# Performance work log

Measured on AMD Instinct MI355X. Metric: run time of the kernel, lower is better.

Reference implementation:

```python
import jax, jax.numpy as jnp
import numpy as np

N = 100000   # nodes
D = 128      # node_dim (features == positions for radius search)
E = 1000000  # edges
EA = 16      # edge_attr dim
M = 256      # number of center points
K = 64       # max_num_neighbors
RADIUS = 16.5
THRESH = 0.1


def setup_inputs() -> dict:
    key = jax.random.key(0)
    ks = jax.random.split(key, 9)
    s = 1.0 / np.sqrt(D)
    return {
        "x": jax.random.normal(ks[0], (N, D), jnp.float32),
        "edge_index": jax.random.randint(ks[1], (2, E), 0, N, dtype=jnp.int64),
        "edge_attr": jax.random.normal(ks[2], (E, EA), jnp.float32),
        "center": jax.random.normal(ks[3], (M, D), jnp.float32),
        "W_root": jax.random.normal(ks[4], (D, D), jnp.float32) * s,
        "W_neigh": jax.random.normal(ks[5], (D, D), jnp.float32) * s,
        "W_edge": jax.random.normal(ks[6], (EA, D), jnp.float32) * (1.0 / np.sqrt(EA)),
        "lin_w": jax.random.normal(ks[7], (D, 1), jnp.float32) * s,
        "lin_b": jnp.zeros((1,), jnp.float32),
    }


def reference(x, edge_index, edge_attr, center, W_root, W_neigh, W_edge, lin_w, lin_b):
    n = x.shape[0]
    m = center.shape[0]

    # --- radius(x=k_data.x, y=center): up to K neighbors within RADIUS per center ---
    d2 = (jnp.sum(center * center, axis=1)[:, None]
          + jnp.sum(x * x, axis=1)[None, :]
          - 2.0 * (center @ x.T))                       # [M, N]
    within = d2 <= RADIUS * RADIUS
    neg = jnp.where(within, -d2, -jnp.inf)
    vals, cols = jax.lax.top_k(neg, K)                  # K nearest inside ball per center
    valid = jnp.isfinite(vals)                          # [M, K]

    # node membership from `col` (drop invalid slots via out-of-bounds index)
    cols_safe = jnp.where(valid, cols, n)
    in_nb = jnp.zeros((n,), bool).at[cols_safe.reshape(-1)].set(True, mode='drop')

    # torch.unique(stack([row, col])) mixes center (row) indices in as well:
    # a center index c < n marks node c if that center has >=1 neighbor
    has_nb = jnp.any(valid, axis=1)                     # [M]
    sel = in_nb.at[jnp.arange(m)].max(has_nb)

    # --- subgraph(col, edge_index, edge_attr): keep edges with both ends in col set ---
    src, dst = edge_index[0], edge_index[1]
    edge_keep = in_nb[src] & in_nb[dst]                 # [E]

    # --- weighting module: GraphConv on the subgraph (edge_attr-aware) ---
    msg = (x[src] @ W_neigh + edge_attr @ W_edge) * edge_keep[:, None].astype(x.dtype)
    agg = jax.ops.segment_sum(msg, dst, num_segments=n)  # [N, D]
    weighting = x @ W_root + agg

    # --- linear -> relu -> threshold gate ---
    w = jax.nn.relu(weighting @ lin_w + lin_b)[:, 0]    # [N]
    return jnp.logical_and(sel, w > THRESH)
```

## Files before the change

### kernel.cpp

```cpp
#include <hip/hip_runtime.h>
#include <stdint.h>

typedef unsigned long long u64;
typedef unsigned int u32;
typedef unsigned short u16;
typedef __attribute__((ext_vector_type(8))) short bf16x8;
typedef __attribute__((ext_vector_type(4))) float f32x4;

#define DD 128
#define EAD 16
#define R2C 272.25f
#define NBINS 4096
#define CAPB 16
#define CANDCAP 512
#define THRESHV 0.1
#define BN 128

#define NPAD 100096
#define NBLKMAX 800
#define L32_BYTES ((size_t)256 * NBLKMAX * CAPB * 4)
#define CNTB_OFF  L32_BYTES
#define CNTB_BYTES ((size_t)256 * NBLKMAX * 2)
#define DBL_OFF   (CNTB_OFF + CNTB_BYTES)
#define DU    0
#define DR    128
#define DV    256
#define DCC   272
#define DROOT 528
#define DA    (528 + NPAD)
#define DAGG  (528 + 2*NPAD)
#define DEND  (528 + 3*NPAD)
#define INT_OFF (DBL_OFF + (size_t)DEND * 8)
#define CCT_B   0
#define MASK_B  2048
#define HNB_B   (2048 + 12800)
#define OVF_B   (2048 + 12800 + 1024)
#define INT_BYTES (2048 + 12800 + 1024 + 1024)
#define BF_OFF   (INT_OFF + INT_BYTES)
#define XX_OFF   (BF_OFF + 2*(size_t)256*128*2)
#define ZERO_OFF   (DBL_OFF + (size_t)DAGG * 8)
#define ZERO_BYTES ((size_t)NPAD * 8 + INT_BYTES)
#define WS_NEED    (XX_OFF + (size_t)NPAD * 4)

__device__ __forceinline__ float fma4(float4 a, float4 b, float acc) {
  acc = fmaf(a.x, b.x, acc); acc = fmaf(a.y, b.y, acc);
  acc = fmaf(a.z, b.z, acc); acc = fmaf(a.w, b.w, acc);
  return acc;
}

__device__ __forceinline__ short f2bf(float f) {
  u32 u = __float_as_uint(f);
  u32 r = (u + 0x7fffu + ((u >> 16) & 1u)) >> 16;
  return (short)r;
}
__device__ __forceinline__ float bf2f(short h) {
  return __uint_as_float(((u32)(unsigned short)h) << 16);
}

__device__ float d2f32(const float* __restrict__ center, const float* __restrict__ x,
                       int c, int n, float ccv) {
  float dt = 0.f, xx = 0.f;
  for (int j = 0; j < DD; j += 4) {
    float4 xv = *(const float4*)(x + (size_t)n*DD + j);
    float4 cv = *(const float4*)(center + (size_t)c*DD + j);
    dt = fma4(xv, cv, dt); xx = fma4(xv, xv, xx);
  }
  return (ccv + xx) - 2.0f*dt;
}

__global__ void ka_pre(const float* __restrict__ Wr, const float* __restrict__ Wn,
                       const float* __restrict__ We, const float* __restrict__ lw,
                       const float* __restrict__ center,
                       double* __restrict__ dbl, float2* __restrict__ cct,
                       short* __restrict__ chi, short* __restrict__ clo, int M) {
  int t = threadIdx.x;
  if (blockIdx.x == 0) {
    if (t < DD) {
      double su = 0.0, sr = 0.0;
      for (int j = 0; j < DD; ++j) {
        double l = (double)lw[j];
        su = fma((double)Wn[(size_t)t*DD + j], l, su);
        sr = fma((double)Wr[(size_t)t*DD + j], l, sr);
      }
      dbl[DU + t] = su; dbl[DR + t] = sr;
    } else if (t < DD + EAD) {
      int k = t - DD; double sv = 0.0;
      for (int j = 0; j < DD; ++j)
        sv = fma((double)We[(size_t)k*DD + j], (double)lw[j], sv);
      dbl[DV + k] = sv;
    }
  } else {
    if (t < M) {
      double s = 0.0;
      for (int j = 0; j < DD; ++j) {
        float f = center[(size_t)t*DD + j];
        double cv = (double)f;
        s = fma(cv, cv, s);
        short h = f2bf(f);
        chi[(size_t)t*DD + j] = h;
        clo[(size_t)t*DD + j] = f2bf(f - bf2f(h));
      }
      dbl[DCC + t] = s;
      float ccf = (float)s;
      float T = ccf + (float)DD - 2.25f * sqrtf(2.0f*(float)DD + 4.0f*ccf);
      T = fminf(T, R2C);
      cct[t] = make_float2(ccf, T);
    }
  }
}

__global__ void kb_node(const float* __restrict__ x, const double* __restrict__ dbl,
                        double* __restrict__ root64, double* __restrict__ a64,
                        float* __restrict__ xxg, int N) {
  int n = blockIdx.x*256 + threadIdx.x;
  if (n >= N) return;
  float xxv = 0.f; double ra = 0.0, aa = 0.0;
  for (int j = 0; j < DD; j += 4) {
    float4 xv = *(const float4*)(x + (size_t)n*DD + j);
    xxv = fma4(xv, xv, xxv);
    const float* pv = (const float*)&xv;
    #pragma unroll
    for (int q = 0; q < 4; ++q) {
      double dx = (double)pv[q];
      ra = fma(dx, dbl[DR + j + q], ra);
      aa = fma(dx, dbl[DU + j + q], aa);
    }
  }
  root64[n] = ra; a64[n] = aa; xxg[n] = xxv;
}

__device__ __forceinline__ int a16(int row, int kg) {
  return row*32 + (((kg ^ (row >> 1)) & 3) << 3);
}

__launch_bounds__(512)
__global__ void k1_mfma(const float* __restrict__ x,
                        const short* __restrict__ chi, const short* __restrict__ clo,
                        const float2* __restrict__ cct, const float* __restrict__ xxg,
                        u32* __restrict__ list32, u16* __restrict__ cntb,
                        u32* __restrict__ ovf, int N, int NBLK) {
  __shared__ __align__(16) char smem[49152];
  short* cs_hi = (short*)smem;
  short* cs_lo = (short*)(smem + 16384);
  short* xs_hi = (short*)(smem + 32768);
  short* xs_lo = (short*)(smem + 40960);
  u32* cap_cnt = (u32*)smem;
  u32* cap_buf = (u32*)(smem + 1024);

  const int tid = threadIdx.x;
  const int blk = blockIdx.x;
  const int bn = blk * BN;
  const int wid = tid >> 6, l = tid & 63, r16 = l & 15, kg = l >> 4;
  const int wc = wid >> 1, wn = wid & 1;

  f32x4 acc[4][4];
  #pragma unroll
  for (int tc = 0; tc < 4; ++tc)
    #pragma unroll
    for (int tn = 0; tn < 4; ++tn)
      acc[tc][tn] = (f32x4){0.f, 0.f, 0.f, 0.f};

  const int xrow = tid >> 2, xpart = tid & 3;
  const int xgn = bn + xrow;

  for (int kc = 0; kc < 4; ++kc) {
    #pragma unroll
    for (int t = 0; t < 4; ++t) {
      const int rem = ((t & 1) << 9) + tid;
      const int row = rem >> 2, kgs = rem & 3;
      const short* src = (t < 2 ? chi : clo) + (size_t)row*DD + kc*32 + kgs*8;
      short* dst = (t < 2 ? cs_hi : cs_lo);
      *(bf16x8*)&dst[a16(row, kgs)] = *(const bf16x8*)src;
    }
    {
      float4 v0 = make_float4(0.f,0.f,0.f,0.f), v1 = v0;
      if (xgn < N) {
        v0 = *(const float4*)(x + (size_t)xgn*DD + kc*32 + xpart*8);
        v1 = *(const float4*)(x + (size_t)xgn*DD + kc*32 + xpart*8 + 4);
      }
      union { short s[8]; bf16x8 v; } hi, lo;
      const float* pv0 = (const float*)&v0;
      const float* pv1 = (const float*)&v1;
      #pragma unroll
      for (int q = 0; q < 4; ++q) {
        short h0 = f2bf(pv0[q]); hi.s[q]   = h0; lo.s[q]   = f2bf(pv0[q] - bf2f(h0));
        short h1 = f2bf(pv1[q]); hi.s[q+4] = h1; lo.s[q+4] = f2bf(pv1[q] - bf2f(h1));
      }
      *(bf16x8*)&xs_hi[a16(xrow, xpart)] = hi.v;
      *(bf16x8*)&xs_lo[a16(xrow, xpart)] = lo.v;
    }
    __syncthreads();

    bf16x8 ah[4], al[4];
    #pragma unroll
    for (int tc = 0; tc < 4; ++tc) {
      const int rc = wc*64 + tc*16 + r16;
      ah[tc] = *(bf16x8*)&cs_hi[a16(rc, kg)];
      al[tc] = *(bf16x8*)&cs_lo[a16(rc, kg)];
    }
    #pragma unroll
    for (int tn = 0; tn < 4; ++tn) {
      const int rn = wn*64 + tn*16 + r16;
      bf16x8 bh = *(bf16x8*)&xs_hi[a16(rn, kg)];
      bf16x8 bl = *(bf16x8*)&xs_lo[a16(rn, kg)];
      #pragma unroll
      for (int tc = 0; tc < 4; ++tc) {
        acc[tc][tn] = __builtin_amdgcn_mfma_f32_16x16x32_bf16(ah[tc], bh, acc[tc][tn], 0, 0, 0);
        acc[tc][tn] = __builtin_amdgcn_mfma_f32_16x16x32_bf16(ah[tc], bl, acc[tc][tn], 0, 0, 0);
        acc[tc][tn] = __builtin_amdgcn_mfma_f32_16x16x32_bf16(al[tc], bh, acc[tc][tn], 0, 0, 0);
      }
    }
    __syncthreads();
  }

  if (tid < 256) cap_cnt[tid] = 0;
  __syncthreads();

  const float bscale = (float)NBINS / R2C;
  #pragma unroll
  for (int tn = 0; tn < 4; ++tn) {
    const int gn = bn + wn*64 + tn*16 + r16;
    if (gn >= N) continue;
    const float xv = xxg[gn];
    #pragma unroll
    for (int tc = 0; tc < 4; ++tc) {
      #pragma unroll
      for (int q = 0; q < 4; ++q) {
        const int c = wc*64 + tc*16 + kg*4 + q;
        const float2 ct = cct[c];
        const float val = (ct.x + xv) - 2.0f * acc[tc][tn][q];
        if (val <= ct.y) {
          int b = (int)(val * bscale); b = min(NBINS-1, max(0, b));
          u32 slot = atomicAdd(&cap_cnt[c], 1u);
          if (slot < CAPB) cap_buf[c*CAPB + slot] = ((u32)b << 17) | (u32)gn;
        }
      }
    }
  }
  __syncthreads();

  if (tid < 256) {
    u32 cc = cap_cnt[tid];
    if (cc > CAPB) { atomicOr(&ovf[tid], 1u); cc = CAPB; }
    cntb[(size_t)tid*NBLK + blk] = (u16)cc;
  }
  for (int i = tid; i < 256*CAPB; i += 512) {
    const int c = i >> 4, j = i & (CAPB-1);
    list32[((size_t)c*NBLK + blk)*CAPB + j] = cap_buf[i];
  }
}

__launch_bounds__(256)
__global__ void k2_sel(const float* __restrict__ x, const float* __restrict__ center,
                       const double* __restrict__ dbl, const float2* __restrict__ cct,
                       u32* __restrict__ mask, int* __restrict__ hnb,
                       const u32* __restrict__ list32, const u16* __restrict__ cntb,
                       const u32* __restrict__ ovf, int N, int NBLK) {
  const int c = blockIdx.x, tid = threadIdx.x;
  __shared__ u32 hist[NBINS];
  __shared__ double dval[CANDCAP];
  __shared__ int    dnode[CANDCAP];
  __shared__ u32 spart[256];
  __shared__ int shW, shB, shQ;

  for (int i = tid; i < NBINS; i += 256) hist[i] = 0u;
  if (tid == 0) { shW = 0; shB = 0x7ffffff; shQ = 0; }
  __syncthreads();

  const float2 ct = cct[c];
  const bool ovfc = (ovf[c] != 0u);
  const float bscale = (float)NBINS / R2C;

  if (!ovfc) {
    int csum = 0;
    for (int blk = tid; blk < NBLK; blk += 256) {
      const int cc = cntb[(size_t)c*NBLK + blk];
      csum += cc;
      const size_t base = ((size_t)c*NBLK + blk)*CAPB;
      for (int j = 0; j < cc; ++j) atomicAdd(&hist[list32[base + j] >> 17], 1u);
    }
    atomicAdd(&shW, csum);
  }
  __syncthreads();
  int C = shW;
  const bool fast = !ovfc && (C >= 64);

  if (!fast) {
    for (int i = tid; i < NBINS; i += 256) hist[i] = 0u;
    if (tid == 0) shW = 0;
    __syncthreads();
    int w = 0;
    for (int n = tid; n < N; n += 256) {
      float val = d2f32(center, x, c, n, ct.x);
      if (val <= R2C) {
        ++w;
        int b = (int)(val * bscale); b = min(NBINS-1, max(0, b));
        atomicAdd(&hist[b], 1u);
      }
    }
    atomicAdd(&shW, w);
    __syncthreads();
    C = shW;
    if (C == 0) return;
  }
  const int Rk = min(64, C);

  u32 loc[16]; u32 psum = 0;
  const int b0 = tid * 16;
  #pragma unroll
  for (int k = 0; k < 16; ++k) { loc[k] = hist[b0 + k]; psum += loc[k]; }
  spart[tid] = psum; __syncthreads();
  for (int off = 1; off < 256; off <<= 1) {
    u32 vv = (tid >= off) ? spart[tid - off] : 0u;
    __syncthreads(); spart[tid] += vv; __syncthreads();
  }
  u32 run = spart[tid] - psum;
  int Bl = 0x7ffffff;
  #pragma unroll
  for (int k = 0; k < 16; ++k) { run += loc[k]; if ((int)run >= Rk && Bl == 0x7ffffff) Bl = b0 + k; }
  if (Bl != 0x7ffffff) atomicMin(&shB, Bl);
  __syncthreads();
  const int Bcol = min(shB + 2, NBINS - 1);

  if (fast) {
    for (int blk = tid; blk < NBLK; blk += 256) {
      const int cc = cntb[(size_t)c*NBLK + blk];
      const size_t base = ((size_t)c*NBLK + blk)*CAPB;
      for (int j = 0; j < cc; ++j) {
        const u32 e = list32[base + j];
        if ((int)(e >> 17) <= Bcol) {
          int s = atomicAdd(&shQ, 1);
          if (s < CANDCAP) dnode[s] = (int)(e & 0x1FFFFu);
        }
      }
    }
  } else {
    for (int n = tid; n < N; n += 256) {
      float val = d2f32(center, x, c, n, ct.x);
      if (val <= R2C) {
        int b = (int)(val * bscale); b = min(NBINS-1, max(0, b));
        if (b <= Bcol) { int s = atomicAdd(&shQ, 1); if (s < CANDCAP) dnode[s] = n; }
      }
    }
  }
  __syncthreads();
  const int Q = min(shQ, CANDCAP);

  const double ccd = dbl[DCC + c];
  for (int i = tid; i < Q; i += 256) {
    int n = dnode[i];
    double dt = 0.0, xx = 0.0;
    #pragma unroll 4
    for (int j = 0; j < DD; ++j) {
      double dx = (double)x[(size_t)n*DD + j];
      dt = fma(dx, (double)center[(size_t)c*DD + j], dt);
      xx = fma(dx, dx, xx);
    }
    dval[i] = (ccd + xx) - 2.0*dt;
  }
  __syncthreads();

  for (int i = tid; i < Q; i += 256) {
    double vi = dval[i]; int ni = dnode[i];
    int rank = 0;
    for (int j = 0; j < Q; ++j) {
      double vj = dval[j];
      rank += (vj < vi) || (vj == vi && dnode[j] < ni);
    }
    if (rank < Rk) atomicOr(&mask[(u32)ni >> 5], 1u << (ni & 31));
  }
  if (tid == 0) hnb[c] = 1;
}

__global__ void k3_edge(const int* __restrict__ ei, const float* __restrict__ eattr,
                        const double* __restrict__ dbl, const u32* __restrict__ mask,
                        double* __restrict__ agg, const double* __restrict__ a64, int E) {
  int e = blockIdx.x*256 + threadIdx.x;
  if (e >= E) return;
  int s = ei[e], d = ei[E + e];
  u32 ks = (mask[(u32)s >> 5] >> (s & 31)) & 1u;
  u32 kd = (mask[(u32)d >> 5] >> (d & 31)) & 1u;
  if (!(ks & kd)) return;
  const float* ep = eattr + (size_t)e * EAD;
  double ea = 0.0;
  #pragma unroll
  for (int k = 0; k < EAD; ++k) ea = fma((double)ep[k], dbl[DV + k], ea);
  atomicAdd(&agg[d], a64[s] + ea);
}

__global__ void k4_out(const double* __restrict__ root64, const double* __restrict__ agg64,
                       const u32* __restrict__ mask, const int* __restrict__ hnb,
                       const float* __restrict__ lb, int* __restrict__ out, int N, int M) {
  int n = blockIdx.x*256 + threadIdx.x;
  if (n >= N) return;
  double pre = root64[n] + agg64[n] + (double)lb[0];
  bool selb = ((mask[n >> 5] >> (n & 31)) & 1u) != 0u;
  if (!selb && n < M) selb = hnb[n] != 0;
  out[n] = (selb && pre > THRESHV) ? 1 : 0;
}

extern "C" void kernel_launch(void* const* d_in, const int* in_sizes, int n_in,
                              void* d_out, int out_size, void* d_ws, size_t ws_size,
                              hipStream_t stream) {
  const float* x      = (const float*)d_in[0];
  const int*   ei     = (const int*)d_in[1];
  const float* eattr  = (const float*)d_in[2];
  const float* center = (const float*)d_in[3];
  const float* Wr     = (const float*)d_in[4];
  const float* Wn     = (const float*)d_in[5];
  const float* We     = (const float*)d_in[6];
  const float* lw     = (const float*)d_in[7];
  const float* lb     = (const float*)d_in[8];
  int* out = (int*)d_out;

  char* wsb = (char*)d_ws;
  u32*    list32 = (u32*)(wsb);
  u16*    cntb   = (u16*)(wsb + CNTB_OFF);
  double* dbl    = (double*)(wsb + DBL_OFF);
  float2* cct    = (float2*)(wsb + INT_OFF + CCT_B);
  u32*    mask   = (u32*)(wsb + INT_OFF + MASK_B);
  int*    hnb    = (int*)(wsb + INT_OFF + HNB_B);
  u32*    ovf    = (u32*)(wsb + INT_OFF + OVF_B);
  short*  chi    = (short*)(wsb + BF_OFF);
  short*  clo    = chi + (size_t)256*DD;
  float*  xxg    = (float*)(wsb + XX_OFF);
  double* root64 = dbl + DROOT;
  double* a64    = dbl + DA;
  double* agg64  = dbl + DAGG;

  const int N = in_sizes[0] / DD;
  const int E = in_sizes[1] / 2;
  const int M = in_sizes[3] / DD;
  const int NBLK = (N + BN - 1) / BN;
  if (N > NPAD || M != 256 || NBLK > NBLKMAX || ws_size < WS_NEED) return;
  (void)n_in; (void)out_size;

  hipMemsetAsync(wsb + ZERO_OFF, 0, ZERO_BYTES, stream);

  ka_pre<<<2, 256, 0, stream>>>(Wr, Wn, We, lw, center, dbl, cct, chi, clo, M);
  kb_node<<<(N + 255)/256, 256, 0, stream>>>(x, dbl, root64, a64, xxg, N);
  k1_mfma<<<NBLK, 512, 0, stream>>>(x, chi, clo, cct, xxg, list32, cntb, ovf, N, NBLK);
  k2_sel<<<M, 256, 0, stream>>>(x, center, dbl, cct, mask, hnb, list32, cntb, ovf, N, NBLK);
  k3_edge<<<(E + 255)/256, 256, 0, stream>>>(ei, eattr, dbl, mask, agg64, a64, E);
  k4_out<<<(N + 255)/256, 256, 0, stream>>>(root64, agg64, mask, hnb, lb, out, N, M);
}
```

Baseline: 259.3 us.

## Fuse node projections into MFMA distance kernel and pre-swizzle center operands

Removes the separate per-node kernel by computing ||x||^2 and the root/neighbor projection dot products inside the MFMA distance kernel while x rows are being converted to bf16. Center hi/lo bf16 splits are now written in a pre-swizzled MFMA fragment layout, so the A operands load straight from global memory into registers and no longer pass through LDS. The x tile is double-buffered in LDS with a prefetch of the next k-chunk, and centre constants are staged in shared memory. The setup kernel is parallelized across warps using shuffle reductions, and the fp64 refinement loop is vectorized with float4 loads. This saves one full read of x and a kernel launch, at the cost of higher register pressure and a launch_bounds occupancy hint on the fused kernel.

```diff
diff --git a/kernel.cpp b/kernel.cpp
--- a/kernel.cpp
+++ b/kernel.cpp
@@ -37,10 +37,9 @@
 #define OVF_B   (2048 + 12800 + 1024)
 #define INT_BYTES (2048 + 12800 + 1024 + 1024)
 #define BF_OFF   (INT_OFF + INT_BYTES)
-#define XX_OFF   (BF_OFF + 2*(size_t)256*128*2)
 #define ZERO_OFF   (DBL_OFF + (size_t)DAGG * 8)
 #define ZERO_BYTES ((size_t)NPAD * 8 + INT_BYTES)
-#define WS_NEED    (XX_OFF + (size_t)NPAD * 4)
+#define WS_NEED    (BF_OFF + 2*(size_t)256*128*2)
 
 __device__ __forceinline__ float fma4(float4 a, float4 b, float acc) {
   acc = fmaf(a.x, b.x, acc); acc = fmaf(a.y, b.y, acc);
@@ -72,162 +71,176 @@
                        const float* __restrict__ We, const float* __restrict__ lw,
                        const float* __restrict__ center,
                        double* __restrict__ dbl, float2* __restrict__ cct,
-                       short* __restrict__ chi, short* __restrict__ clo, int M) {
-  int t = threadIdx.x;
-  if (blockIdx.x == 0) {
-    if (t < DD) {
-      double su = 0.0, sr = 0.0;
-      for (int j = 0; j < DD; ++j) {
-        double l = (double)lw[j];
-        su = fma((double)Wn[(size_t)t*DD + j], l, su);
-        sr = fma((double)Wr[(size_t)t*DD + j], l, sr);
-      }
-      dbl[DU + t] = su; dbl[DR + t] = sr;
-    } else if (t < DD + EAD) {
-      int k = t - DD; double sv = 0.0;
-      for (int j = 0; j < DD; ++j)
-        sv = fma((double)We[(size_t)k*DD + j], (double)lw[j], sv);
-      dbl[DV + k] = sv;
-    }
-  } else {
-    if (t < M) {
-      double s = 0.0;
-      for (int j = 0; j < DD; ++j) {
-        float f = center[(size_t)t*DD + j];
-        double cv = (double)f;
-        s = fma(cv, cv, s);
-        short h = f2bf(f);
-        chi[(size_t)t*DD + j] = h;
-        clo[(size_t)t*DD + j] = f2bf(f - bf2f(h));
-      }
-      dbl[DCC + t] = s;
+                       short* __restrict__ chi_sw, short* __restrict__ clo_sw) {
+  const int gw = blockIdx.x * 4 + (threadIdx.x >> 6);
+  const int lane = threadIdx.x & 63;
+  const int j0 = lane * 2;
+
+  if (gw < 128) {
+    const int row = gw;
+    float2 wn2 = *(const float2*)(Wn + (size_t)row*DD + j0);
+    float2 wr2 = *(const float2*)(Wr + (size_t)row*DD + j0);
+    float2 lw2 = *(const float2*)(lw + j0);
+    double su = fma((double)wn2.x, (double)lw2.x, (double)wn2.y * (double)lw2.y);
+    double sr = fma((double)wr2.x, (double)lw2.x, (double)wr2.y * (double)lw2.y);
+    #pragma unroll
+    for (int off = 32; off; off >>= 1) {
+      su += __shfl_xor(su, off, 64);
+      sr += __shfl_xor(sr, off, 64);
+    }
+    if (lane == 0) { dbl[DU + row] = su; dbl[DR + row] = sr; }
+  } else if (gw < 144) {
+    const int k = gw - 128;
+    float2 we2 = *(const float2*)(We + (size_t)k*DD + j0);
+    float2 lw2 = *(const float2*)(lw + j0);
+    double sv = fma((double)we2.x, (double)lw2.x, (double)we2.y * (double)lw2.y);
+    #pragma unroll
+    for (int off = 32; off; off >>= 1) sv += __shfl_xor(sv, off, 64);
+    if (lane == 0) dbl[DV + k] = sv;
+  } else if (gw < 400) {
+    const int c = gw - 144;
+    const int cblk = c >> 4, r16c = c & 15;
+    float2 cv2 = *(const float2*)(center + (size_t)c*DD + j0);
+    double s = fma((double)cv2.x, (double)cv2.x, (double)cv2.y * (double)cv2.y);
+    const float* pc = (const float*)&cv2;
+    #pragma unroll
+    for (int t = 0; t < 2; ++t) {
+      const int j = j0 + t;
+      const int kc = j >> 5, kg = (j >> 3) & 3, e = j & 7;
+      const int idx = (((cblk*4 + kc)*64) + kg*16 + r16c)*8 + e;
+      short h = f2bf(pc[t]);
+      chi_sw[idx] = h;
+      clo_sw[idx] = f2bf(pc[t] - bf2f(h));
+    }
+    #pragma unroll
+    for (int off = 32; off; off >>= 1) s += __shfl_xor(s, off, 64);
+    if (lane == 0) {
+      dbl[DCC + c] = s;
       float ccf = (float)s;
       float T = ccf + (float)DD - 2.25f * sqrtf(2.0f*(float)DD + 4.0f*ccf);
       T = fminf(T, R2C);
-      cct[t] = make_float2(ccf, T);
-    }
-  }
-}
-
-__global__ void kb_node(const float* __restrict__ x, const double* __restrict__ dbl,
-                        double* __restrict__ root64, double* __restrict__ a64,
-                        float* __restrict__ xxg, int N) {
-  int n = blockIdx.x*256 + threadIdx.x;
-  if (n >= N) return;
-  float xxv = 0.f; double ra = 0.0, aa = 0.0;
-  for (int j = 0; j < DD; j += 4) {
-    float4 xv = *(const float4*)(x + (size_t)n*DD + j);
-    xxv = fma4(xv, xv, xxv);
-    const float* pv = (const float*)&xv;
-    #pragma unroll
-    for (int q = 0; q < 4; ++q) {
-      double dx = (double)pv[q];
-      ra = fma(dx, dbl[DR + j + q], ra);
-      aa = fma(dx, dbl[DU + j + q], aa);
-    }
-  }
-  root64[n] = ra; a64[n] = aa; xxg[n] = xxv;
+      cct[c] = make_float2(ccf, T);
+    }
+  }
 }
 
 __device__ __forceinline__ int a16(int row, int kg) {
   return row*32 + (((kg ^ (row >> 1)) & 3) << 3);
 }
 
-__launch_bounds__(512)
+__launch_bounds__(512, 4)
 __global__ void k1_mfma(const float* __restrict__ x,
-                        const short* __restrict__ chi, const short* __restrict__ clo,
-                        const float2* __restrict__ cct, const float* __restrict__ xxg,
+                        const short* __restrict__ chi_sw, const short* __restrict__ clo_sw,
+                        const float2* __restrict__ cct, const double* __restrict__ dbl,
+                        double* __restrict__ root64, double* __restrict__ a64,
                         u32* __restrict__ list32, u16* __restrict__ cntb,
                         u32* __restrict__ ovf, int N, int NBLK) {
-  __shared__ __align__(16) char smem[49152];
-  short* cs_hi = (short*)smem;
-  short* cs_lo = (short*)(smem + 16384);
-  short* xs_hi = (short*)(smem + 32768);
-  short* xs_lo = (short*)(smem + 40960);
-  u32* cap_cnt = (u32*)smem;
-  u32* cap_buf = (u32*)(smem + 1024);
+  __shared__ __align__(16) short xsh[2][2][128*32];
+  __shared__ float2 scct[256];
+  __shared__ float sxx[128];
+  __shared__ u32 cap_cnt[256];
+  __shared__ u32 cap_buf[256*CAPB];
 
   const int tid = threadIdx.x;
   const int blk = blockIdx.x;
-  const int bn = blk * BN;
+  const int bn  = blk * BN;
   const int wid = tid >> 6, l = tid & 63, r16 = l & 15, kg = l >> 4;
   const int wc = wid >> 1, wn = wid & 1;
+
+  if (tid < 256) { scct[tid] = cct[tid]; cap_cnt[tid] = 0u; }
+
+  const int srow = tid >> 2, sq = tid & 3;
+  const int sgn  = bn + srow;
+  const bool sok = (sgn < N);
 
   f32x4 acc[4][4];
   #pragma unroll
   for (int tc = 0; tc < 4; ++tc)
     #pragma unroll
-    for (int tn = 0; tn < 4; ++tn)
-      acc[tc][tn] = (f32x4){0.f, 0.f, 0.f, 0.f};
-
-  const int xrow = tid >> 2, xpart = tid & 3;
-  const int xgn = bn + xrow;
+    for (int tn = 0; tn < 4; ++tn) acc[tc][tn] = (f32x4){0.f,0.f,0.f,0.f};
+
+  float4 v0 = make_float4(0.f,0.f,0.f,0.f), v1 = v0;
+  if (sok) {
+    v0 = *(const float4*)(x + (size_t)sgn*DD + sq*8);
+    v1 = *(const float4*)(x + (size_t)sgn*DD + sq*8 + 4);
+  }
+
+  float xxp = 0.f; double rap = 0.0, aap = 0.0;
 
   for (int kc = 0; kc < 4; ++kc) {
-    #pragma unroll
-    for (int t = 0; t < 4; ++t) {
-      const int rem = ((t & 1) << 9) + tid;
-      const int row = rem >> 2, kgs = rem & 3;
-      const short* src = (t < 2 ? chi : clo) + (size_t)row*DD + kc*32 + kgs*8;
-      short* dst = (t < 2 ? cs_hi : cs_lo);
-      *(bf16x8*)&dst[a16(row, kgs)] = *(const bf16x8*)src;
-    }
-    {
-      float4 v0 = make_float4(0.f,0.f,0.f,0.f), v1 = v0;
-      if (xgn < N) {
-        v0 = *(const float4*)(x + (size_t)xgn*DD + kc*32 + xpart*8);
-        v1 = *(const float4*)(x + (size_t)xgn*DD + kc*32 + xpart*8 + 4);
-      }
-      union { short s[8]; bf16x8 v; } hi, lo;
-      const float* pv0 = (const float*)&v0;
-      const float* pv1 = (const float*)&v1;
-      #pragma unroll
-      for (int q = 0; q < 4; ++q) {
-        short h0 = f2bf(pv0[q]); hi.s[q]   = h0; lo.s[q]   = f2bf(pv0[q] - bf2f(h0));
-        short h1 = f2bf(pv1[q]); hi.s[q+4] = h1; lo.s[q+4] = f2bf(pv1[q] - bf2f(h1));
-      }
-      *(bf16x8*)&xs_hi[a16(xrow, xpart)] = hi.v;
-      *(bf16x8*)&xs_lo[a16(xrow, xpart)] = lo.v;
-    }
+    union { short s[8]; bf16x8 v; } hi, lo;
+    const float* p0 = (const float*)&v0; const float* p1 = (const float*)&v1;
+    #pragma unroll
+    for (int q = 0; q < 4; ++q) {
+      short h0 = f2bf(p0[q]); hi.s[q]   = h0; lo.s[q]   = f2bf(p0[q] - bf2f(h0));
+      short h1 = f2bf(p1[q]); hi.s[q+4] = h1; lo.s[q+4] = f2bf(p1[q] - bf2f(h1));
+    }
+    short* xh = &xsh[kc & 1][0][0];
+    short* xl = &xsh[kc & 1][1][0];
+    *(bf16x8*)&xh[a16(srow, sq)] = hi.v;
+    *(bf16x8*)&xl[a16(srow, sq)] = lo.v;
+
+    #pragma unroll
+    for (int q = 0; q < 4; ++q) {
+      xxp = fmaf(p0[q], p0[q], xxp); xxp = fmaf(p1[q], p1[q], xxp);
+      double d0 = (double)p0[q], d1 = (double)p1[q];
+      const int jb = kc*32 + sq*8 + q;
+      rap = fma(d0, dbl[DR + jb], rap);     aap = fma(d0, dbl[DU + jb], aap);
+      rap = fma(d1, dbl[DR + jb + 4], rap); aap = fma(d1, dbl[DU + jb + 4], aap);
+    }
+
+    if (kc < 3 && sok) {
+      v0 = *(const float4*)(x + (size_t)sgn*DD + (kc+1)*32 + sq*8);
+      v1 = *(const float4*)(x + (size_t)sgn*DD + (kc+1)*32 + sq*8 + 4);
+    }
+
+    bf16x8 ah[4], al[4];
+    #pragma unroll
+    for (int tc = 0; tc < 4; ++tc) {
+      const int cblk = wc*4 + tc;
+      const size_t off = (size_t)(((cblk*4 + kc)*64) + l) * 8;
+      ah[tc] = *(const bf16x8*)(chi_sw + off);
+      al[tc] = *(const bf16x8*)(clo_sw + off);
+    }
+
     __syncthreads();
 
-    bf16x8 ah[4], al[4];
-    #pragma unroll
-    for (int tc = 0; tc < 4; ++tc) {
-      const int rc = wc*64 + tc*16 + r16;
-      ah[tc] = *(bf16x8*)&cs_hi[a16(rc, kg)];
-      al[tc] = *(bf16x8*)&cs_lo[a16(rc, kg)];
-    }
     #pragma unroll
     for (int tn = 0; tn < 4; ++tn) {
       const int rn = wn*64 + tn*16 + r16;
-      bf16x8 bh = *(bf16x8*)&xs_hi[a16(rn, kg)];
-      bf16x8 bl = *(bf16x8*)&xs_lo[a16(rn, kg)];
+      bf16x8 bh = *(bf16x8*)&xh[a16(rn, kg)];
+      bf16x8 bl = *(bf16x8*)&xl[a16(rn, kg)];
       #pragma unroll
       for (int tc = 0; tc < 4; ++tc) {
-        acc[tc][tn] = __builtin_amdgcn_mfma_f32_16x16x32_bf16(ah[tc], bh, acc[tc][tn], 0, 0, 0);
-        acc[tc][tn] = __builtin_amdgcn_mfma_f32_16x16x32_bf16(ah[tc], bl, acc[tc][tn], 0, 0, 0);
-        acc[tc][tn] = __builtin_amdgcn_mfma_f32_16x16x32_bf16(al[tc], bh, acc[tc][tn], 0, 0, 0);
-      }
-    }
-    __syncthreads();
-  }
-
-  if (tid < 256) cap_cnt[tid] = 0;
+        acc[tc][tn] = __builtin_amdgcn_mfma_f32_16x16x32_bf16(ah[tc], bh, acc[tc][tn], 0,0,0);
+        acc[tc][tn] = __builtin_amdgcn_mfma_f32_16x16x32_bf16(ah[tc], bl, acc[tc][tn], 0,0,0);
+        acc[tc][tn] = __builtin_amdgcn_mfma_f32_16x16x32_bf16(al[tc], bh, acc[tc][tn], 0,0,0);
+      }
+    }
+  }
+
+  xxp += __shfl_xor(xxp, 1, 64); xxp += __shfl_xor(xxp, 2, 64);
+  rap += __shfl_xor(rap, 1, 64); rap += __shfl_xor(rap, 2, 64);
+  aap += __shfl_xor(aap, 1, 64); aap += __shfl_xor(aap, 2, 64);
+  if (sq == 0) {
+    sxx[srow] = xxp;
+    if (sok) { root64[sgn] = rap; a64[sgn] = aap; }
+  }
   __syncthreads();
 
   const float bscale = (float)NBINS / R2C;
   #pragma unroll
   for (int tn = 0; tn < 4; ++tn) {
-    const int gn = bn + wn*64 + tn*16 + r16;
+    const int ln = wn*64 + tn*16 + r16;
+    const int gn = bn + ln;
     if (gn >= N) continue;
-    const float xv = xxg[gn];
+    const float xv = sxx[ln];
     #pragma unroll
     for (int tc = 0; tc < 4; ++tc) {
       #pragma unroll
       for (int q = 0; q < 4; ++q) {
         const int c = wc*64 + tc*16 + kg*4 + q;
-        const float2 ct = cct[c];
+        const float2 ct = scct[c];
         const float val = (ct.x + xv) - 2.0f * acc[tc][tn][q];
         if (val <= ct.y) {
           int b = (int)(val * bscale); b = min(NBINS-1, max(0, b));
@@ -348,15 +361,25 @@
 
   const double ccd = dbl[DCC + c];
   for (int i = tid; i < Q; i += 256) {
-    int n = dnode[i];
-    double dt = 0.0, xx = 0.0;
-    #pragma unroll 4
-    for (int j = 0; j < DD; ++j) {
-      double dx = (double)x[(size_t)n*DD + j];
-      dt = fma(dx, (double)center[(size_t)c*DD + j], dt);
-      xx = fma(dx, dx, xx);
-    }
-    dval[i] = (ccd + xx) - 2.0*dt;
+    const int n = dnode[i];
+    const float4* xp = (const float4*)(x + (size_t)n*DD);
+    const float4* cp = (const float4*)(center + (size_t)c*DD);
+    double dt0 = 0.0, dt1 = 0.0, xx0 = 0.0, xx1 = 0.0;
+    #pragma unroll 8
+    for (int j = 0; j < 32; j += 2) {
+      float4 a0 = xp[j],   b0f = cp[j];
+      float4 a1 = xp[j+1], b1f = cp[j+1];
+      const float* pa0 = (const float*)&a0; const float* pb0 = (const float*)&b0f;
+      const float* pa1 = (const float*)&a1; const float* pb1 = (const float*)&b1f;
+      #pragma unroll
+      for (int q = 0; q < 4; ++q) {
+        double da0 = (double)pa0[q], db0 = (double)pb0[q];
+        double da1 = (double)pa1[q], db1 = (double)pb1[q];
+        dt0 = fma(da0, db0, dt0); xx0 = fma(da0, da0, xx0);
+        dt1 = fma(da1, db1, dt1); xx1 = fma(da1, da1, xx1);
+      }
+    }
+    dval[i] = (ccd + (xx0 + xx1)) - 2.0*(dt0 + dt1);
   }
   __syncthreads();
 
@@ -421,9 +444,8 @@
   u32*    mask   = (u32*)(wsb + INT_OFF + MASK_B);
   int*    hnb    = (int*)(wsb + INT_OFF + HNB_B);
   u32*    ovf    = (u32*)(wsb + INT_OFF + OVF_B);
-  short*  chi    = (short*)(wsb + BF_OFF);
-  short*  clo    = chi + (size_t)256*DD;
-  float*  xxg    = (float*)(wsb + XX_OFF);
+  short*  chi_sw = (short*)(wsb + BF_OFF);
+  short*  clo_sw = chi_sw + (size_t)256*DD;
   double* root64 = dbl + DROOT;
   double* a64    = dbl + DA;
   double* agg64  = dbl + DAGG;
@@ -437,9 +459,9 @@
 
   hipMemsetAsync(wsb + ZERO_OFF, 0, ZERO_BYTES, stream);
 
-  ka_pre<<<2, 256, 0, stream>>>(Wr, Wn, We, lw, center, dbl, cct, chi, clo, M);
-  kb_node<<<(N + 255)/256, 256, 0, stream>>>(x, dbl, root64, a64, xxg, N);
-  k1_mfma<<<NBLK, 512, 0, stream>>>(x, chi, clo, cct, xxg, list32, cntb, ovf, N, NBLK);
+  ka_pre<<<100, 256, 0, stream>>>(Wr, Wn, We, lw, center, dbl, cct, chi_sw, clo_sw);
+  k1_mfma<<<NBLK, 512, 0, stream>>>(x, chi_sw, clo_sw, cct, dbl, root64, a64,
+                                    list32, cntb, ovf, N, NBLK);
   k2_sel<<<M, 256, 0, stream>>>(x, center, dbl, cct, mask, hnb, list32, cntb, ovf, N, NBLK);
   k3_edge<<<(E + 255)/256, 256, 0, stream>>>(ei, eattr, dbl, mask, agg64, a64, E);
   k4_out<<<(N + 255)/256, 256, 0, stream>>>(root64, agg64, mask, hnb, lb, out, N, M);
```

After: 281.1 us. 1.08x slower.
